# Kernel tuning notes

Hardware: AMD Instinct MI355X
Metric: run time of the kernel (lower is better)

The kernel has to match this reference:

```python
import jax, jax.numpy as jnp
import numpy as np

N_ATOMS = 500000
N_BONDS = 1000000
MAX_NB = 6
ATOM_FDIM = 133
BOND_FDIM = 14
HIDDEN = 128
MP_DEPTH = 3
ATOMS_PER_MOL = 20


def setup_inputs() -> dict:
    key = jax.random.key(0)
    ks = jax.random.split(key, 12)
    inp = {
        "f_atoms": jax.random.normal(ks[0], (N_ATOMS, ATOM_FDIM), jnp.float32),
        "f_bonds": jax.random.normal(ks[1], (N_BONDS, BOND_FDIM), jnp.float32),
        "Wi_w": jax.random.normal(ks[2], (HIDDEN, ATOM_FDIM), jnp.float32) * 0.05,
        "Wi_b": jax.random.normal(ks[3], (HIDDEN,), jnp.float32) * 0.05,
        "Wh_w": jax.random.normal(ks[4], (HIDDEN, HIDDEN + BOND_FDIM), jnp.float32) * 0.05,
        "Wh_b": jax.random.normal(ks[5], (HIDDEN,), jnp.float32) * 0.05,
        "Wo_w": jax.random.normal(ks[6], (HIDDEN, ATOM_FDIM + HIDDEN), jnp.float32) * 0.05,
        "Wo_b": jax.random.normal(ks[7], (HIDDEN,), jnp.float32) * 0.05,
        "ffn_w": jax.random.normal(ks[8], (1, HIDDEN), jnp.float32) * 0.05,
        "ffn_b": jax.random.normal(ks[9], (1,), jnp.float32) * 0.05,
        "a2a": jax.random.randint(ks[10], (N_ATOMS, MAX_NB), 0, N_ATOMS, jnp.int32),
        "a2b": jax.random.randint(ks[11], (N_ATOMS, MAX_NB), 0, N_BONDS, jnp.int32),
        "atoms_per_mol": ATOMS_PER_MOL,
    }
    return inp


def reference(f_atoms, f_bonds, Wi_w, Wi_b, Wh_w, Wh_b, Wo_w, Wo_b, ffn_w, ffn_b,
              a2a, a2b, atoms_per_mol):
    # W_i + ReLU: initial atom messages
    x = f_atoms @ Wi_w.T + Wi_b                     # [N_atoms, H]
    message = jax.nn.relu(x)
    # pre-aggregate bond features once (constant across depths)
    nei_f_bonds_sum = f_bonds[a2b].sum(axis=1)      # [N_atoms, BOND_FDIM]
    for _ in range(MP_DEPTH - 1):
        # gather neighbor messages and sum (index_select_ND + sum(dim=1));
        # concat(msg_gather, bond_gather).sum(1) == concat(sum(msg), sum(bond))
        nei_a_message = message[a2a].sum(axis=1)    # [N_atoms, H]
        nei = jnp.concatenate([nei_a_message, nei_f_bonds_sum], axis=1)
        message = jax.nn.relu(x + nei @ Wh_w.T + Wh_b)
        # dropout is identity in eval mode
    # final aggregation + W_o
    a_message = message[a2a].sum(axis=1)            # [N_atoms, H]
    a_input = jnp.concatenate([f_atoms, a_message], axis=1)
    atom_hiddens = jax.nn.relu(a_input @ Wo_w.T + Wo_b)
    # max readout per molecule (equal-size a_scope of atoms_per_mol)
    n_atoms, h = atom_hiddens.shape
    mol_vecs = atom_hiddens.reshape(n_atoms // atoms_per_mol, atoms_per_mol, h).max(axis=1)
    # FFN head (NN_depth=1): Dropout (identity) + Linear(H -> 1)
    return mol_vecs @ ffn_w.T + ffn_b               # [n_mols, 1]
```

## Files before the change

kernel.cpp:

```cpp
#include <hip/hip_runtime.h>
#include <hip/hip_bf16.h>

#define N_ATOMS   500000
#define N_BONDS   1000000
#define MAX_NB    6
#define ATOM_FDIM 133
#define BOND_FDIM 14
#define HIDDEN    128
#define N_MOLS    25000
#define APM       20

typedef __attribute__((ext_vector_type(8))) short short8;
typedef __attribute__((ext_vector_type(4))) float f32x4;
typedef unsigned short u16;
typedef unsigned int   u32;

__device__ __forceinline__ float bf2f(u16 u) {
    u32 t = ((u32)u) << 16;
    return __builtin_bit_cast(float, t);
}
__device__ __forceinline__ u16 f2bf(float f) {
    u32 t = __builtin_bit_cast(u32, f);
    t += 0x7FFFu + ((t >> 16) & 1u);
    return (u16)(t >> 16);
}

__global__ void prep_weights(const float* __restrict__ Wi, const float* __restrict__ Wh,
                             const float* __restrict__ Wo,
                             u16* __restrict__ Wip, u16* __restrict__ Whp, u16* __restrict__ Wop) {
    int stride = gridDim.x * blockDim.x;
    int tid = blockIdx.x * blockDim.x + threadIdx.x;
    for (int i = tid; i < 128 * 160; i += stride) {
        int r = i / 160, c = i % 160;
        Wip[i] = (c < 133) ? f2bf(Wi[r * 133 + c]) : (u16)0;
        Whp[i] = (c < 142) ? f2bf(Wh[r * 142 + c]) : (u16)0;
    }
    for (int i = tid; i < 128 * 288; i += stride) {
        int r = i / 288, c = i % 288;
        float v = 0.f;
        if (c < 133)      v = Wo[r * 261 + c];
        else if (c >= 160) v = Wo[r * 261 + (c - 27)];
        Wop[i] = f2bf(v);
    }
}

__global__ __launch_bounds__(256) void fa_convert(const float* __restrict__ fa, u16* __restrict__ out) {
    long t = (long)blockIdx.x * 256 + threadIdx.x;
    if (t >= (long)N_ATOMS * 20) return;
    int row = (int)(t / 20);
    int c8  = (int)(t % 20) * 8;
    const float* src = fa + (long)row * ATOM_FDIM;
    u16 u[8];
#pragma unroll
    for (int e = 0; e < 8; e++) {
        int c = c8 + e;
        u[e] = (c < ATOM_FDIM) ? f2bf(src[c]) : (u16)0;
    }
    uint4 v;
    v.x = (u32)u[0] | ((u32)u[1] << 16);
    v.y = (u32)u[2] | ((u32)u[3] << 16);
    v.z = (u32)u[4] | ((u32)u[5] << 16);
    v.w = (u32)u[6] | ((u32)u[7] << 16);
    *(uint4*)(out + (long)row * 160 + c8) = v;
}

__global__ __launch_bounds__(256) void bond_gather(const float* __restrict__ fb, const int* __restrict__ a2b,
                                                   u16* __restrict__ outp) {
    long t = (long)blockIdx.x * 256 + threadIdx.x;
    int atom = (int)(t >> 4);
    int c2   = (int)(t & 15);
    if (atom >= N_ATOMS) return;
    int c0 = 2 * c2, c1 = c0 + 1;
    float s0 = 0.f, s1 = 0.f;
    if (c0 < BOND_FDIM) {
#pragma unroll
        for (int j = 0; j < MAX_NB; j++) {
            int idx = a2b[atom * 6 + j];
            const float* row = fb + (long)idx * BOND_FDIM;
            s0 += row[c0];
            if (c1 < BOND_FDIM) s1 += row[c1];
        }
    }
    *(u32*)(outp + (long)atom * 32 + c0) = (u32)f2bf(s0) | ((u32)f2bf(s1) << 16);
}

__global__ __launch_bounds__(256) void gather_relu_sum(const u16* __restrict__ src,
                                                       const int* __restrict__ a2a,
                                                       u16* __restrict__ dst) {
    long t = (long)blockIdx.x * 256 + threadIdx.x;
    int atom = (int)(t >> 4);
    int c8   = (int)(t & 15) << 3;
    float s[8] = {0, 0, 0, 0, 0, 0, 0, 0};
#pragma unroll
    for (int j = 0; j < MAX_NB; j++) {
        int idx = a2a[atom * 6 + j];
        uint4 v = *(const uint4*)(src + (long)idx * 128 + c8);
        u32 w[4] = {v.x, v.y, v.z, v.w};
#pragma unroll
        for (int q = 0; q < 4; q++) {
            s[2 * q]     += fmaxf(bf2f((u16)(w[q] & 0xFFFFu)), 0.f);
            s[2 * q + 1] += fmaxf(bf2f((u16)(w[q] >> 16)), 0.f);
        }
    }
    uint4 o;
    o.x = (u32)f2bf(s[0]) | ((u32)f2bf(s[1]) << 16);
    o.y = (u32)f2bf(s[2]) | ((u32)f2bf(s[3]) << 16);
    o.z = (u32)f2bf(s[4]) | ((u32)f2bf(s[5]) << 16);
    o.w = (u32)f2bf(s[6]) | ((u32)f2bf(s[7]) << 16);
    *(uint4*)(dst + (long)atom * 128 + c8) = o;
}

template <int KB0, int KB1, bool ADDX>
__global__ __launch_bounds__(512, 4) void gemm_mp(const u16* __restrict__ A0, int ldA0,
                                                  const u16* __restrict__ A1, int ldA1,
                                                  const u16* __restrict__ Wp,
                                                  const float* __restrict__ bias,
                                                  const u16* __restrict__ Xadd,
                                                  u16* __restrict__ Out) {
    constexpr int KB  = KB0 + KB1;
    constexpr int KP  = KB * 32;
    constexpr int LDW = KP + 8;
    __shared__ u16 ldsw[128 * LDW];
    for (int i = threadIdx.x; i < 128 * (KP / 8); i += 512) {
        int r  = i / (KP / 8);
        int c8 = (i % (KP / 8)) * 8;
        *(uint4*)(&ldsw[r * LDW + c8]) = *(const uint4*)(Wp + r * KP + c8);
    }
    __syncthreads();

    const int lane = threadIdx.x & 63;
    const int wave = threadIdx.x >> 6;
    const int lrow = lane & 15;
    const int kg   = lane >> 4;
    const long rowbase = (long)blockIdx.x * 256 + wave * 32;

    f32x4 acc[2][8];
#pragma unroll
    for (int m = 0; m < 2; m++)
#pragma unroll
        for (int n = 0; n < 8; n++) acc[m][n] = (f32x4){0.f, 0.f, 0.f, 0.f};

    long ar[2];
#pragma unroll
    for (int m = 0; m < 2; m++) {
        long r = rowbase + m * 16 + lrow;
        if (r >= N_ATOMS) r = N_ATOMS - 1;
        ar[m] = r;
    }

#pragma unroll
    for (int kb = 0; kb < KB; kb++) {
        const u16* As;
        int ld, koff;
        if (kb < KB0) { As = A0; ld = ldA0; koff = kb * 32; }
        else          { As = A1; ld = ldA1; koff = (kb - KB0) * 32; }
        short8 af[2];
#pragma unroll
        for (int m = 0; m < 2; m++)
            af[m] = __builtin_bit_cast(short8, *(const uint4*)(As + ar[m] * ld + koff + kg * 8));
#pragma unroll
        for (int n = 0; n < 8; n++) {
            short8 bf = __builtin_bit_cast(short8, *(const uint4*)(&ldsw[(n * 16 + lrow) * LDW + kb * 32 + kg * 8]));
            acc[0][n] = __builtin_amdgcn_mfma_f32_16x16x32_bf16(bf, af[0], acc[0][n], 0, 0, 0);
            acc[1][n] = __builtin_amdgcn_mfma_f32_16x16x32_bf16(bf, af[1], acc[1][n], 0, 0, 0);
        }
    }

#pragma unroll
    for (int m = 0; m < 2; m++) {
        long r = rowbase + m * 16 + lrow;
        if (r >= N_ATOMS) continue;
#pragma unroll
        for (int n = 0; n < 8; n++) {
            int c0 = n * 16 + kg * 4;
            float4 b4 = *(const float4*)(bias + c0);
            float v0 = acc[m][n][0] + b4.x;
            float v1 = acc[m][n][1] + b4.y;
            float v2 = acc[m][n][2] + b4.z;
            float v3 = acc[m][n][3] + b4.w;
            if (ADDX) {
                uint2 xv = *(const uint2*)(Xadd + r * 128 + c0);
                v0 += bf2f((u16)(xv.x & 0xFFFFu));
                v1 += bf2f((u16)(xv.x >> 16));
                v2 += bf2f((u16)(xv.y & 0xFFFFu));
                v3 += bf2f((u16)(xv.y >> 16));
            }
            uint2 o;
            o.x = (u32)f2bf(v0) | ((u32)f2bf(v1) << 16);
            o.y = (u32)f2bf(v2) | ((u32)f2bf(v3) << 16);
            *(uint2*)(Out + r * 128 + c0) = o;
        }
    }
}

__global__ __launch_bounds__(256) void readout(const u16* __restrict__ ah,
                                               const float* __restrict__ ffn_w,
                                               const float* __restrict__ ffn_b,
                                               float* __restrict__ out) {
    int mol  = blockIdx.x * 4 + (threadIdx.x >> 6);
    int lane = threadIdx.x & 63;
    if (mol >= N_MOLS) return;
    float m0 = -1e30f, m1 = -1e30f;
    const u16* base = ah + (long)mol * APM * 128 + 2 * lane;
#pragma unroll
    for (int a = 0; a < APM; a++) {
        u32 v = *(const u32*)(base + a * 128);
        m0 = fmaxf(m0, bf2f((u16)(v & 0xFFFFu)));
        m1 = fmaxf(m1, bf2f((u16)(v >> 16)));
    }
    m0 = fmaxf(m0, 0.f);
    m1 = fmaxf(m1, 0.f);
    float p = m0 * ffn_w[2 * lane] + m1 * ffn_w[2 * lane + 1];
#pragma unroll
    for (int off = 32; off > 0; off >>= 1) p += __shfl_down(p, off);
    if (lane == 0) out[mol] = p + ffn_b[0];
}

extern "C" void kernel_launch(void* const* d_in, const int* in_sizes, int n_in,
                              void* d_out, int out_size, void* d_ws, size_t ws_size,
                              hipStream_t stream) {
    const float* f_atoms = (const float*)d_in[0];
    const float* f_bonds = (const float*)d_in[1];
    const float* Wi_w = (const float*)d_in[2];
    const float* Wi_b = (const float*)d_in[3];
    const float* Wh_w = (const float*)d_in[4];
    const float* Wh_b = (const float*)d_in[5];
    const float* Wo_w = (const float*)d_in[6];
    const float* Wo_b = (const float*)d_in[7];
    const float* ffn_w = (const float*)d_in[8];
    const float* ffn_b = (const float*)d_in[9];
    const int* a2a = (const int*)d_in[10];
    const int* a2b = (const int*)d_in[11];
    float* out = (float*)d_out;

    char* ws = (char*)d_ws;
    u16* fa    = (u16*)(ws);
    u16* xb    = (u16*)(ws + 160000000L);
    u16* msg   = (u16*)(ws + 288000000L);
    u16* nsum  = (u16*)(ws + 416000000L);
    u16* nbond = (u16*)(ws + 544000000L);
    u16* Wip   = (u16*)(ws + 576000000L);
    u16* Whp   = (u16*)(ws + 576040960L);
    u16* Wop   = (u16*)(ws + 576081920L);

    prep_weights<<<64, 256, 0, stream>>>(Wi_w, Wh_w, Wo_w, Wip, Whp, Wop);
    fa_convert<<<39063, 256, 0, stream>>>(f_atoms, fa);
    bond_gather<<<31250, 256, 0, stream>>>(f_bonds, a2b, nbond);

    gemm_mp<5, 0, false><<<1954, 512, 0, stream>>>(fa, 160, (const u16*)nullptr, 0, Wip, Wi_b, (const u16*)nullptr, xb);

    gather_relu_sum<<<31250, 256, 0, stream>>>(xb, a2a, nsum);
    gemm_mp<4, 1, true><<<1954, 512, 0, stream>>>(nsum, 128, nbond, 32, Whp, Wh_b, xb, msg);
    gather_relu_sum<<<31250, 256, 0, stream>>>(msg, a2a, nsum);
    gemm_mp<4, 1, true><<<1954, 512, 0, stream>>>(nsum, 128, nbond, 32, Whp, Wh_b, xb, msg);
    gather_relu_sum<<<31250, 256, 0, stream>>>(msg, a2a, nsum);
    gemm_mp<5, 4, false><<<1954, 512, 0, stream>>>(fa, 160, nsum, 128, Wop, Wo_b, (const u16*)nullptr, msg);

    readout<<<6250, 256, 0, stream>>>(msg, ffn_w, ffn_b, out);
}
```

Measured before the change: 1.012 ms.

## Fuse neighbor gather-relu-sum into message-passing GEMM and stage atom conversion via LDS

The separate gather_relu_sum kernel is removed. Each GEMM block now gathers its rows' six neighbor messages, applies ReLU and sums them in registers before the MFMA loop, so the nsum intermediate is never written to or read back from global memory. The GEMM is re-tiled to 256 threads and 128 rows per block, with A operands and the x residual prefetched into registers, and messages ping-pong between two buffers. fa_convert now stages rows through LDS for coalesced float4 loads. The trade-off is much higher register pressure and random gathers that the MFMA work may no longer hide.

```diff
diff --git a/kernel.cpp b/kernel.cpp
--- a/kernel.cpp
+++ b/kernel.cpp
@@ -44,24 +44,34 @@
     }
 }
 
+#define CROWS 24
 __global__ __launch_bounds__(256) void fa_convert(const float* __restrict__ fa, u16* __restrict__ out) {
-    long t = (long)blockIdx.x * 256 + threadIdx.x;
-    if (t >= (long)N_ATOMS * 20) return;
-    int row = (int)(t / 20);
-    int c8  = (int)(t % 20) * 8;
-    const float* src = fa + (long)row * ATOM_FDIM;
-    u16 u[8];
-#pragma unroll
-    for (int e = 0; e < 8; e++) {
-        int c = c8 + e;
-        u[e] = (c < ATOM_FDIM) ? f2bf(src[c]) : (u16)0;
-    }
-    uint4 v;
-    v.x = (u32)u[0] | ((u32)u[1] << 16);
-    v.y = (u32)u[2] | ((u32)u[3] << 16);
-    v.z = (u32)u[4] | ((u32)u[5] << 16);
-    v.w = (u32)u[6] | ((u32)u[7] << 16);
-    *(uint4*)(out + (long)row * 160 + c8) = v;
+    __shared__ float buf[CROWS * 133];
+    const long row0 = (long)blockIdx.x * CROWS;
+    const int rows = (int)((N_ATOMS - row0) < CROWS ? (N_ATOMS - row0) : CROWS);
+    const float* src = fa + row0 * ATOM_FDIM;
+    if (rows == CROWS) {
+        for (int i = threadIdx.x; i < (CROWS * 133) / 4; i += 256)
+            *(float4*)(&buf[i * 4]) = *(const float4*)(src + i * 4);
+    } else {
+        for (int i = threadIdx.x; i < rows * 133; i += 256) buf[i] = src[i];
+    }
+    __syncthreads();
+    for (int j = threadIdx.x; j < rows * 20; j += 256) {
+        int r = j / 20, c8 = (j % 20) * 8;
+        u16 u[8];
+#pragma unroll
+        for (int e = 0; e < 8; e++) {
+            int c = c8 + e;
+            u[e] = (c < ATOM_FDIM) ? f2bf(buf[r * 133 + c]) : (u16)0;
+        }
+        uint4 v;
+        v.x = (u32)u[0] | ((u32)u[1] << 16);
+        v.y = (u32)u[2] | ((u32)u[3] << 16);
+        v.z = (u32)u[4] | ((u32)u[5] << 16);
+        v.w = (u32)u[6] | ((u32)u[7] << 16);
+        *(uint4*)(out + (row0 + r) * 160 + c8) = v;
+    }
 }
 
 __global__ __launch_bounds__(256) void bond_gather(const float* __restrict__ fb, const int* __restrict__ a2b,
@@ -84,61 +94,23 @@
     *(u32*)(outp + (long)atom * 32 + c0) = (u32)f2bf(s0) | ((u32)f2bf(s1) << 16);
 }
 
-__global__ __launch_bounds__(256) void gather_relu_sum(const u16* __restrict__ src,
-                                                       const int* __restrict__ a2a,
-                                                       u16* __restrict__ dst) {
-    long t = (long)blockIdx.x * 256 + threadIdx.x;
-    int atom = (int)(t >> 4);
-    int c8   = (int)(t & 15) << 3;
-    float s[8] = {0, 0, 0, 0, 0, 0, 0, 0};
-#pragma unroll
-    for (int j = 0; j < MAX_NB; j++) {
-        int idx = a2a[atom * 6 + j];
-        uint4 v = *(const uint4*)(src + (long)idx * 128 + c8);
-        u32 w[4] = {v.x, v.y, v.z, v.w};
-#pragma unroll
-        for (int q = 0; q < 4; q++) {
-            s[2 * q]     += fmaxf(bf2f((u16)(w[q] & 0xFFFFu)), 0.f);
-            s[2 * q + 1] += fmaxf(bf2f((u16)(w[q] >> 16)), 0.f);
-        }
-    }
-    uint4 o;
-    o.x = (u32)f2bf(s[0]) | ((u32)f2bf(s[1]) << 16);
-    o.y = (u32)f2bf(s[2]) | ((u32)f2bf(s[3]) << 16);
-    o.z = (u32)f2bf(s[4]) | ((u32)f2bf(s[5]) << 16);
-    o.w = (u32)f2bf(s[6]) | ((u32)f2bf(s[7]) << 16);
-    *(uint4*)(dst + (long)atom * 128 + c8) = o;
-}
-
-template <int KB0, int KB1, bool ADDX>
-__global__ __launch_bounds__(512, 4) void gemm_mp(const u16* __restrict__ A0, int ldA0,
-                                                  const u16* __restrict__ A1, int ldA1,
-                                                  const u16* __restrict__ Wp,
-                                                  const float* __restrict__ bias,
-                                                  const u16* __restrict__ Xadd,
-                                                  u16* __restrict__ Out) {
-    constexpr int KB  = KB0 + KB1;
+template <int KB0, int KBG, int KB1, bool ADDX, int MINW>
+__global__ __launch_bounds__(256, MINW) void gemm_fused(
+    const u16* __restrict__ A0, int ldA0,
+    const u16* __restrict__ Gsrc, const int* __restrict__ a2a,
+    const u16* __restrict__ A1, int ldA1,
+    const u16* __restrict__ Wp, const float* __restrict__ bias,
+    const u16* __restrict__ Xadd, u16* __restrict__ Out) {
+    constexpr int KB  = KB0 + KBG + KB1;
     constexpr int KP  = KB * 32;
     constexpr int LDW = KP + 8;
     __shared__ u16 ldsw[128 * LDW];
-    for (int i = threadIdx.x; i < 128 * (KP / 8); i += 512) {
-        int r  = i / (KP / 8);
-        int c8 = (i % (KP / 8)) * 8;
-        *(uint4*)(&ldsw[r * LDW + c8]) = *(const uint4*)(Wp + r * KP + c8);
-    }
-    __syncthreads();
 
     const int lane = threadIdx.x & 63;
     const int wave = threadIdx.x >> 6;
     const int lrow = lane & 15;
     const int kg   = lane >> 4;
-    const long rowbase = (long)blockIdx.x * 256 + wave * 32;
-
-    f32x4 acc[2][8];
-#pragma unroll
-    for (int m = 0; m < 2; m++)
-#pragma unroll
-        for (int n = 0; n < 8; n++) acc[m][n] = (f32x4){0.f, 0.f, 0.f, 0.f};
+    const long rowbase = (long)blockIdx.x * 128 + wave * 32;
 
     long ar[2];
 #pragma unroll
@@ -148,16 +120,81 @@
         ar[m] = r;
     }
 
+    short8 agf[2][KBG ? KBG : 1];
+    if constexpr (KBG > 0) {
+#pragma unroll
+        for (int m = 0; m < 2; m++) {
+            const int* ip = a2a + ar[m] * 6;
+            int idx[6];
+#pragma unroll
+            for (int j = 0; j < 6; j++) idx[j] = ip[j];
+            uint4 g[6][KBG];
+#pragma unroll
+            for (int j = 0; j < 6; j++) {
+                const u16* s = Gsrc + (long)idx[j] * 128 + kg * 8;
+#pragma unroll
+                for (int kb = 0; kb < KBG; kb++) g[j][kb] = *(const uint4*)(s + kb * 32);
+            }
+#pragma unroll
+            for (int kb = 0; kb < KBG; kb++) {
+                float s[8] = {0, 0, 0, 0, 0, 0, 0, 0};
+#pragma unroll
+                for (int j = 0; j < 6; j++) {
+                    u32 w4[4] = {g[j][kb].x, g[j][kb].y, g[j][kb].z, g[j][kb].w};
+#pragma unroll
+                    for (int q = 0; q < 4; q++) {
+                        s[2 * q]     += fmaxf(__builtin_bit_cast(float, w4[q] << 16), 0.f);
+                        s[2 * q + 1] += fmaxf(__builtin_bit_cast(float, w4[q] & 0xFFFF0000u), 0.f);
+                    }
+                }
+                uint4 pk;
+                pk.x = (u32)f2bf(s[0]) | ((u32)f2bf(s[1]) << 16);
+                pk.y = (u32)f2bf(s[2]) | ((u32)f2bf(s[3]) << 16);
+                pk.z = (u32)f2bf(s[4]) | ((u32)f2bf(s[5]) << 16);
+                pk.w = (u32)f2bf(s[6]) | ((u32)f2bf(s[7]) << 16);
+                agf[m][kb] = __builtin_bit_cast(short8, pk);
+            }
+        }
+    }
+
+    for (int i = threadIdx.x; i < 128 * (KP / 8); i += 256) {
+        int r  = i / (KP / 8);
+        int c8 = (i % (KP / 8)) * 8;
+        *(uint4*)(&ldsw[r * LDW + c8]) = *(const uint4*)(Wp + r * KP + c8);
+    }
+    __syncthreads();
+
+    uint4 a0v[2][KB0 ? KB0 : 1];
+    uint4 a1v[2][KB1 ? KB1 : 1];
+#pragma unroll
+    for (int m = 0; m < 2; m++) {
+        if constexpr (KB0 > 0) {
+            const u16* p0 = A0 + ar[m] * ldA0 + kg * 8;
+#pragma unroll
+            for (int kb = 0; kb < KB0; kb++) a0v[m][kb] = *(const uint4*)(p0 + kb * 32);
+        }
+        if constexpr (KB1 > 0) {
+            const u16* p1 = A1 + ar[m] * ldA1 + kg * 8;
+#pragma unroll
+            for (int kb = 0; kb < KB1; kb++) a1v[m][kb] = *(const uint4*)(p1 + kb * 32);
+        }
+    }
+
+    f32x4 acc[2][8];
+#pragma unroll
+    for (int m = 0; m < 2; m++)
+#pragma unroll
+        for (int n = 0; n < 8; n++) acc[m][n] = (f32x4){0.f, 0.f, 0.f, 0.f};
+
 #pragma unroll
     for (int kb = 0; kb < KB; kb++) {
-        const u16* As;
-        int ld, koff;
-        if (kb < KB0) { As = A0; ld = ldA0; koff = kb * 32; }
-        else          { As = A1; ld = ldA1; koff = (kb - KB0) * 32; }
         short8 af[2];
 #pragma unroll
-        for (int m = 0; m < 2; m++)
-            af[m] = __builtin_bit_cast(short8, *(const uint4*)(As + ar[m] * ld + koff + kg * 8));
+        for (int m = 0; m < 2; m++) {
+            if (kb < KB0)            af[m] = __builtin_bit_cast(short8, a0v[m][kb < KB0 ? kb : 0]);
+            else if (kb < KB0 + KBG) af[m] = agf[m][(kb - KB0) < KBG ? (kb - KB0) : 0];
+            else                     af[m] = __builtin_bit_cast(short8, a1v[m][(kb - KB0 - KBG) < KB1 ? (kb - KB0 - KBG) : 0]);
+        }
 #pragma unroll
         for (int n = 0; n < 8; n++) {
             short8 bf = __builtin_bit_cast(short8, *(const uint4*)(&ldsw[(n * 16 + lrow) * LDW + kb * 32 + kg * 8]));
@@ -166,6 +203,18 @@
         }
     }
 
+    uint2 xv[2][8];
+    if constexpr (ADDX) {
+#pragma unroll
+        for (int m = 0; m < 2; m++) {
+            long r = rowbase + m * 16 + lrow;
+            if (r < N_ATOMS) {
+#pragma unroll
+                for (int n = 0; n < 8; n++)
+                    xv[m][n] = *(const uint2*)(Xadd + r * 128 + n * 16 + kg * 4);
+            }
+        }
+    }
 #pragma unroll
     for (int m = 0; m < 2; m++) {
         long r = rowbase + m * 16 + lrow;
@@ -178,12 +227,11 @@
             float v1 = acc[m][n][1] + b4.y;
             float v2 = acc[m][n][2] + b4.z;
             float v3 = acc[m][n][3] + b4.w;
-            if (ADDX) {
-                uint2 xv = *(const uint2*)(Xadd + r * 128 + c0);
-                v0 += bf2f((u16)(xv.x & 0xFFFFu));
-                v1 += bf2f((u16)(xv.x >> 16));
-                v2 += bf2f((u16)(xv.y & 0xFFFFu));
-                v3 += bf2f((u16)(xv.y >> 16));
+            if constexpr (ADDX) {
+                v0 += __builtin_bit_cast(float, xv[m][n].x << 16);
+                v1 += __builtin_bit_cast(float, xv[m][n].x & 0xFFFF0000u);
+                v2 += __builtin_bit_cast(float, xv[m][n].y << 16);
+                v3 += __builtin_bit_cast(float, xv[m][n].y & 0xFFFF0000u);
             }
             uint2 o;
             o.x = (u32)f2bf(v0) | ((u32)f2bf(v1) << 16);
@@ -236,25 +284,27 @@
     char* ws = (char*)d_ws;
     u16* fa    = (u16*)(ws);
     u16* xb    = (u16*)(ws + 160000000L);
-    u16* msg   = (u16*)(ws + 288000000L);
-    u16* nsum  = (u16*)(ws + 416000000L);
+    u16* msgA  = (u16*)(ws + 288000000L);
+    u16* msgB  = (u16*)(ws + 416000000L);
     u16* nbond = (u16*)(ws + 544000000L);
     u16* Wip   = (u16*)(ws + 576000000L);
     u16* Whp   = (u16*)(ws + 576040960L);
     u16* Wop   = (u16*)(ws + 576081920L);
 
     prep_weights<<<64, 256, 0, stream>>>(Wi_w, Wh_w, Wo_w, Wip, Whp, Wop);
-    fa_convert<<<39063, 256, 0, stream>>>(f_atoms, fa);
+    fa_convert<<<(N_ATOMS + CROWS - 1) / CROWS, 256, 0, stream>>>(f_atoms, fa);
     bond_gather<<<31250, 256, 0, stream>>>(f_bonds, a2b, nbond);
 
-    gemm_mp<5, 0, false><<<1954, 512, 0, stream>>>(fa, 160, (const u16*)nullptr, 0, Wip, Wi_b, (const u16*)nullptr, xb);
-
-    gather_relu_sum<<<31250, 256, 0, stream>>>(xb, a2a, nsum);
-    gemm_mp<4, 1, true><<<1954, 512, 0, stream>>>(nsum, 128, nbond, 32, Whp, Wh_b, xb, msg);
-    gather_relu_sum<<<31250, 256, 0, stream>>>(msg, a2a, nsum);
-    gemm_mp<4, 1, true><<<1954, 512, 0, stream>>>(nsum, 128, nbond, 32, Whp, Wh_b, xb, msg);
-    gather_relu_sum<<<31250, 256, 0, stream>>>(msg, a2a, nsum);
-    gemm_mp<5, 4, false><<<1954, 512, 0, stream>>>(fa, 160, nsum, 128, Wop, Wo_b, (const u16*)nullptr, msg);
-
-    readout<<<6250, 256, 0, stream>>>(msg, ffn_w, ffn_b, out);
-}
+    gemm_fused<5, 0, 0, false, 3><<<3907, 256, 0, stream>>>(
+        fa, 160, (const u16*)nullptr, (const int*)nullptr, (const u16*)nullptr, 0,
+        Wip, Wi_b, (const u16*)nullptr, xb);
+
+    gemm_fused<0, 4, 1, true, 3><<<3907, 256, 0, stream>>>(
+        (const u16*)nullptr, 0, xb, a2a, nbond, 32, Whp, Wh_b, xb, msgA);
+    gemm_fused<0, 4, 1, true, 3><<<3907, 256, 0, stream>>>(
+        (const u16*)nullptr, 0, msgA, a2a, nbond, 32, Whp, Wh_b, xb, msgB);
+    gemm_fused<5, 4, 0, false, 2><<<3907, 256, 0, stream>>>(
+        fa, 160, msgB, a2a, (const u16*)nullptr, 0, Wop, Wo_b, (const u16*)nullptr, msgA);
+
+    readout<<<6250, 256, 0, stream>>>(msgA, ffn_w, ffn_b, out);
+}
```

Result: slower. 1.058 ms (+4.5%).
